# Kernel tuning notes

Hardware: AMD Instinct MI355X
Metric: run time of the kernel (lower is better)

Reference implementation:

```python
import jax, jax.numpy as jnp
import numpy as np

VOCAB, EMB, SEQ, BATCH, UNITS = 10000, 100, 80, 128, 1024


def setup_inputs() -> dict:
    key = jax.random.key(0)
    ks = jax.random.split(key, 12)
    s = lambda k, shape, scale: (jax.random.normal(k, shape, dtype=jnp.float32) * scale)
    inp = {
        'tokens': jax.random.randint(ks[0], (BATCH, SEQ), 0, VOCAB, dtype=jnp.int32),
        'E':   s(ks[1], (VOCAB, EMB), 0.05),
        # GRU cell 1 (input dim = EMB)
        'Wx1': s(ks[2], (EMB, 3 * UNITS), 1.0 / np.sqrt(EMB)),
        'Wh1': s(ks[3], (UNITS, 3 * UNITS), 1.0 / np.sqrt(UNITS)),
        'bx1': jnp.zeros((3 * UNITS,), jnp.float32),
        'bh1': jnp.zeros((3 * UNITS,), jnp.float32),
        # GRU cell 2 (input dim = UNITS)
        'Wx2': s(ks[4], (UNITS, 3 * UNITS), 1.0 / np.sqrt(UNITS)),
        'Wh2': s(ks[5], (UNITS, 3 * UNITS), 1.0 / np.sqrt(UNITS)),
        'bx2': jnp.zeros((3 * UNITS,), jnp.float32),
        'bh2': jnp.zeros((3 * UNITS,), jnp.float32),
        # final dense -> 1 with sigmoid
        'Wf':  s(ks[6], (UNITS, 1), 1.0 / np.sqrt(UNITS)),
        'bf':  jnp.zeros((1,), jnp.float32),
    }
    return inp


def _gru_cell(h, x, Wx, Wh, bx, bh):
    # TF2 keras GRUCell, reset_after=True (inference, no dropout)
    gx = x @ Wx + bx            # [B, 3U]
    gh = h @ Wh + bh            # [B, 3U]
    xz, xr, xn = jnp.split(gx, 3, axis=-1)
    hz, hr, hn = jnp.split(gh, 3, axis=-1)
    z = jax.nn.sigmoid(xz + hz)
    r = jax.nn.sigmoid(xr + hr)
    n = jnp.tanh(xn + r * hn)   # reset_after: r applied AFTER recurrent matmul
    return z * h + (1.0 - z) * n


def reference(tokens, E, Wx1, Wh1, bx1, bh1, Wx2, Wh2, bx2, bh2, Wf, bf):
    x = E[tokens]                         # [B, T, EMB]
    xt = jnp.transpose(x, (1, 0, 2))      # [T, B, EMB] for scan over time
    h0 = jnp.zeros((BATCH, UNITS), x.dtype)
    h1 = jnp.zeros((BATCH, UNITS), x.dtype)

    def step(carry, word):
        h0, h1 = carry
        h0 = _gru_cell(h0, word, Wx1, Wh1, bx1, bh1)
        h1 = _gru_cell(h1, h0,   Wx2, Wh2, bx2, bh2)
        return (h0, h1), None

    (h0, h1), _ = jax.lax.scan(step, (h0, h1), xt)
    return jax.nn.sigmoid(h1 @ Wf + bf)   # [B, 1]
```

## Files before the change

### kernel.cpp

```cpp
#include <hip/hip_runtime.h>
#include <hip/hip_bf16.h>

typedef __bf16 bf16;
typedef __bf16 bf16x8 __attribute__((ext_vector_type(8)));
typedef __bf16 bf16x4 __attribute__((ext_vector_type(4)));
typedef float f32x4 __attribute__((ext_vector_type(4)));

#define T_SEQ 80
#define NB 128
#define NT 1024
#define U 1024
#define U3 3072

#define WT_OFF   0ull
#define WXT_OFF  18874368ull
#define XG_OFF   19660800ull
#define GX1_OFF  22282240ull
#define H0B_OFF  85196800ull
#define H1B_OFF  106430464ull
#define CNT_OFF  127664128ull
#define WS_NEED  127666176ull

#define HBUF_ELEMS 131072ull


#define LDS_SX2_OFF   147456
#define LDS_RED_OFF   (147456 + 24*132*4)
#define LDS_BYTES     (LDS_RED_OFF + 64)

__device__ __forceinline__ float sigmoidf_(float x) { return 1.f / (1.f + __expf(-x)); }

__global__ void k_embed(const int* __restrict__ tok, const float* __restrict__ E,
                        bf16* __restrict__ Xg) {
  int idx = blockIdx.x * 256 + threadIdx.x;
  int k = idx & 127;
  int bt = idx >> 7;
  int b = bt & 127;
  int t = bt >> 7;
  float v = 0.f;
  if (k < 100) v = E[(size_t)tok[b * 80 + t] * 100 + k];
  Xg[idx] = (bf16)v;
}

__global__ void k_trans(const float* __restrict__ Wh1, const float* __restrict__ Wx2,
                        const float* __restrict__ Wh2, bf16* __restrict__ WT) {
  __shared__ float tile[32][33];
  const float* src = (blockIdx.z == 0) ? Wh1 : (blockIdx.z == 1) ? Wx2 : Wh2;
  int cb = blockIdx.x * 32, kb = blockIdx.y * 32;
  int tx = threadIdx.x, ty = threadIdx.y;
  for (int i = ty; i < 32; i += 8) tile[i][tx] = src[(size_t)(kb + i) * U3 + cb + tx];
  __syncthreads();
  bf16* dst = WT + (size_t)blockIdx.z * U3 * U;
  for (int i = ty; i < 32; i += 8) dst[(size_t)(cb + i) * U + kb + tx] = (bf16)tile[tx][i];
}

__global__ void k_wxt(const float* __restrict__ Wx1, bf16* __restrict__ WXT) {
  __shared__ float tile[32][33];
  int cb = blockIdx.x * 32, kb = blockIdx.y * 32;
  int tx = threadIdx.x, ty = threadIdx.y;
  for (int i = ty; i < 32; i += 8) {
    int k = kb + i;
    tile[i][tx] = (k < 100) ? Wx1[(size_t)k * U3 + cb + tx] : 0.f;
  }
  __syncthreads();
  for (int i = ty; i < 32; i += 8) WXT[(size_t)(cb + i) * 128 + kb + tx] = (bf16)tile[tx][i];
}

__global__ __launch_bounds__(256) void k_gx1(const bf16* __restrict__ Xg,
                                             const bf16* __restrict__ WXT,
                                             const float* __restrict__ bx1,
                                             bf16* __restrict__ GX1) {
  int mb = blockIdx.x * 64, nb = blockIdx.y * 64;
  int w = threadIdx.x >> 6, l = threadIdx.x & 63;
  int lr = l & 15, lq = l >> 4;
  int rowA = mb + w * 16 + lr;
  int tA = rowA >> 7, bA = rowA & 127;
  const bf16* aptr = Xg + ((size_t)tA * 128 + bA) * 128 + lq * 8;
  f32x4 acc[4] = {};
  #pragma unroll
  for (int ks = 0; ks < 4; ++ks) {
    bf16x8 a = *(const bf16x8*)(aptr + ks * 32);
    #pragma unroll
    for (int nt = 0; nt < 4; ++nt) {
      int col = nb + nt * 16 + lr;
      bf16x8 b = *(const bf16x8*)(WXT + (size_t)col * 128 + ks * 32 + lq * 8);
      acc[nt] = __builtin_amdgcn_mfma_f32_16x16x32_bf16(a, b, acc[nt], 0, 0, 0);
    }
  }
  int m0 = mb + w * 16 + lq * 4;
  int t0 = m0 >> 7, b0 = m0 & 127;
  #pragma unroll
  for (int nt = 0; nt < 4; ++nt) {
    int col = nb + nt * 16 + lr;
    float bias = bx1[col];
    bf16x4 o;
    #pragma unroll
    for (int j = 0; j < 4; ++j) o[j] = (bf16)(acc[nt][j] + bias);
    *(bf16x4*)(GX1 + ((size_t)t0 * U3 + col) * 128 + b0) = o;
  }
}

__device__ __forceinline__ bf16x8 ldsw(const bf16* Wlds, int sid, int k8) {
  return *(const bf16x8*)(Wlds + ((size_t)sid << 10) + ((k8 ^ (sid & 7) ^ (sid & 8)) << 3));
}

__device__ __forceinline__ void st_pair(bf16* dst_even, int lr, float h) {
  bf16 hb16 = (bf16)h;
  unsigned hb = (unsigned)__builtin_bit_cast(unsigned short, hb16);
  unsigned pb = (unsigned)__shfl_xor((int)hb, 1) & 0xffffu;
  if (!(lr & 1)) {
    unsigned v = hb | (pb << 16);
    __hip_atomic_store((unsigned*)dst_even, v, __ATOMIC_RELAXED, __HIP_MEMORY_SCOPE_AGENT);
  }
}

__device__ void gridbar(int* cnt, int i) {
  __syncthreads();
  if (threadIdx.x == 0) {
    int* gc   = cnt + (blockIdx.x & 7) * 32;
    int* root = cnt + 256;
    int* go   = cnt + 288;
    int old = __hip_atomic_fetch_add(gc, 1, __ATOMIC_RELAXED, __HIP_MEMORY_SCOPE_AGENT);
    if (old == 16 * (i + 1) - 1) {
      int r = __hip_atomic_fetch_add(root, 1, __ATOMIC_RELAXED, __HIP_MEMORY_SCOPE_AGENT);
      if (r == 8 * (i + 1) - 1)
        __hip_atomic_store(go, i + 1, __ATOMIC_RELAXED, __HIP_MEMORY_SCOPE_AGENT);
    }
    while (__hip_atomic_load(go, __ATOMIC_RELAXED, __HIP_MEMORY_SCOPE_AGENT) < i + 1)
      __builtin_amdgcn_s_sleep(4);
  }
  __syncthreads();
}

__global__ __launch_bounds__(NT, 1) void k_main(
    const bf16* __restrict__ WT, const bf16* __restrict__ GX1,
    bf16* __restrict__ h0b, bf16* __restrict__ h1b, int* __restrict__ cnt,
    const float* __restrict__ bh1, const float* __restrict__ bx2,
    const float* __restrict__ bh2, const float* __restrict__ Wf,
    const float* __restrict__ bfp, float* __restrict__ out) {
  extern __shared__ char lds[];
  bf16* Wlds = (bf16*)lds;
  float* Sx2 = (float*)(lds + LDS_SX2_OFF);
  float* red = (float*)(lds + LDS_RED_OFF);

  const int tid = threadIdx.x;
  const int w = tid >> 6, l = tid & 63;
  const int lr = l & 15, lq = l >> 4;
  const int c0 = blockIdx.x * 8;
  const int koff = ((blockIdx.x >> 3) & 15) * 2;

  const int wr_kq = (c0 >> 5) * 512 + (c0 & 31);

  for (int u = tid; u < 9216; u += NT) {
    int chunk = u & 127;
    int sid = u >> 7;
    int mat, gcol;
    if (sid < 16)      { mat = 0; gcol = c0 + (sid & 7) + ((sid >> 3) << 10); }
    else if (sid < 32) { int s = sid - 16; mat = 1; gcol = c0 + (s & 7) + ((s >> 3) << 10); }
    else if (sid < 56) { int s = sid - 32; mat = 2; gcol = c0 + (s & 7) + ((s >> 3) << 10); }
    else               { int s = sid - 56; mat = (s < 8) ? 0 : 1; gcol = 2 * U + c0 + (s & 7); }
    bf16x8 v = *(const bf16x8*)(WT + ((size_t)mat * U3 + gcol) * U + chunk * 8);
    *(bf16x8*)(Wlds + ((size_t)sid << 10) + ((chunk ^ (sid & 7) ^ (sid & 8)) << 3)) = v;
  }
  __syncthreads();

  const int zr_idx = (lr < 8) ? (c0 + lr) : (U + c0 + lr - 8);
  const int n_idx = 2 * U + c0 + (lr & 7);
  const float bzr1 = bh1[zr_idx];
  const float bhn1 = bh1[n_idx];
  const float bzr2 = bx2[zr_idx] + bh2[zr_idx];
  const float bxn2 = bx2[n_idx];
  const float bhn2 = bh2[n_idx];

  float hm[4];
  #pragma unroll
  for (int q = 0; q < 4; ++q) hm[q] = 0.f;

  for (int i = 0; i <= T_SEQ; ++i) {
    const bf16* h0r = h0b + (size_t)i * HBUF_ELEMS;
    const bf16* h1r = h1b + (size_t)(i > 0 ? i - 1 : 0) * HBUF_ELEMS;
    bf16* h0w = h0b + (size_t)(i + 1) * HBUF_ELEMS;
    bf16* h1w = h1b + (size_t)i * HBUF_ELEMS;

    f32x4 a3zr = {}, a3n = {};

    if (w < 8) {
      f32x4 a1zr = {}, a2zr = {}, an = {};

      bf16x4 g4p = {}, gnp = {};
      if (i < T_SEQ) {
        const bf16* gx = GX1 + (size_t)i * U3 * 128;
        int r0 = w * 16 + lq * 4;
        g4p = *(const bf16x4*)(gx + (size_t)zr_idx * 128 + r0);
        gnp = *(const bf16x4*)(gx + (size_t)(2 * U + c0 + (lr & 7)) * 128 + r0);
      }

      const bf16* abase = h0r + w * 16384 + lr * 32 + lq * 8;
      #pragma unroll 8
      for (int ks = 0; ks < 32; ++ks) {
        int kss = (ks + koff) & 31;
        bf16x8 A = *(const bf16x8*)(abase + kss * 512);
        int k8 = kss * 4 + lq;
        bf16x8 B1zr = ldsw(Wlds, lr, k8);
        bf16x8 B2zr = ldsw(Wlds, 16 + lr, k8);
        bf16x8 Bn   = ldsw(Wlds, 56 + lr, k8);
        a1zr = __builtin_amdgcn_mfma_f32_16x16x32_bf16(A, B1zr, a1zr, 0, 0, 0);
        a2zr = __builtin_amdgcn_mfma_f32_16x16x32_bf16(A, B2zr, a2zr, 0, 0, 0);
        an   = __builtin_amdgcn_mfma_f32_16x16x32_bf16(A, Bn,   an,   0, 0, 0);
      }
      {
        int r0 = w * 16 + lq * 4;
        *(f32x4*)(Sx2 + lr * 132 + r0) = a2zr;
        if (lr >= 8) *(f32x4*)(Sx2 + (16 + (lr - 8)) * 132 + r0) = an;
      }
      if (i < T_SEQ) {
        f32x4 sv;
        #pragma unroll
        for (int j = 0; j < 4; ++j) sv[j] = sigmoidf_(a1zr[j] + bzr1 + (float)g4p[j]);
        f32x4 rv;
        #pragma unroll
        for (int j = 0; j < 4; ++j) rv[j] = __shfl_xor(sv[j], 8);
        if (lr < 8) {
          #pragma unroll
          for (int j = 0; j < 4; ++j) {
            float nn = tanhf((float)gnp[j] + rv[j] * (an[j] + bhn1));
            float z = sv[j];
            float h = z * hm[j] + (1.f - z) * nn;
            hm[j] = h;
            st_pair(h0w + w * 16384 + wr_kq + (lq * 4 + j) * 32 + (lr & ~1), lr, h);
          }
        }
      }
    } else if (i > 0) {
      const bf16* abase = h1r + (w - 8) * 16384 + lr * 32 + lq * 8;
      #pragma unroll 8
      for (int ks = 0; ks < 32; ++ks) {
        int kss = (ks + koff) & 31;
        bf16x8 A = *(const bf16x8*)(abase + kss * 512);
        int k8 = kss * 4 + lq;
        bf16x8 B3zr = ldsw(Wlds, 32 + lr, k8);
        bf16x8 B3n  = ldsw(Wlds, 48 + (lr & 7), k8);
        a3zr = __builtin_amdgcn_mfma_f32_16x16x32_bf16(A, B3zr, a3zr, 0, 0, 0);
        a3n  = __builtin_amdgcn_mfma_f32_16x16x32_bf16(A, B3n,  a3n, 0, 0, 0);
      }
    }
    __syncthreads();
    if (w >= 8 && i > 0) {
      int r0 = (w - 8) * 16 + lq * 4;
      f32x4 sv;
      #pragma unroll
      for (int j = 0; j < 4; ++j)
        sv[j] = sigmoidf_(a3zr[j] + bzr2 + Sx2[lr * 132 + r0 + j]);
      f32x4 rv;
      #pragma unroll
      for (int j = 0; j < 4; ++j) rv[j] = __shfl_xor(sv[j], 8);
      if (lr < 8) {
        #pragma unroll
        for (int j = 0; j < 4; ++j) {
          float xn = Sx2[(16 + lr) * 132 + r0 + j] + bxn2;
          float nn = tanhf(xn + rv[j] * (a3n[j] + bhn2));
          float z = sv[j];
          float h = z * hm[j] + (1.f - z) * nn;
          hm[j] = h;
          st_pair(h1w + (w - 8) * 16384 + wr_kq + (lq * 4 + j) * 32 + (lr & ~1), lr, h);
        }
      }
    }
    gridbar(cnt, i);
  }

  {
    const bf16* h1f = h1b + (size_t)T_SEQ * HBUF_ELEMS;
    const int b = blockIdx.x;
    float part = 0.f;
    if (tid < 256) {
      int k0 = tid * 4;
      const bf16* p = h1f + (b >> 4) * 16384 + (k0 >> 5) * 512 + (b & 15) * 32 + (k0 & 31);
      bf16x4 hv = *(const bf16x4*)p;
      #pragma unroll
      for (int j = 0; j < 4; ++j) part += (float)hv[j] * Wf[k0 + j];
    }
    #pragma unroll
    for (int off = 32; off > 0; off >>= 1) part += __shfl_down(part, off);
    if (l == 0) red[w] = part;
    __syncthreads();
    if (tid == 0) {
      float s = bfp[0];
      #pragma unroll
      for (int q = 0; q < 16; ++q) s += red[q];
      out[blockIdx.x] = sigmoidf_(s);
    }
  }
}

extern "C" void kernel_launch(void* const* d_in, const int* in_sizes, int n_in,
                              void* d_out, int out_size, void* d_ws, size_t ws_size,
                              hipStream_t stream) {
  if (ws_size < WS_NEED) return;
  const int*   tok = (const int*)d_in[0];
  const float* E   = (const float*)d_in[1];
  const float* Wx1 = (const float*)d_in[2];
  const float* Wh1 = (const float*)d_in[3];
  const float* bx1 = (const float*)d_in[4];
  const float* bh1 = (const float*)d_in[5];
  const float* Wx2 = (const float*)d_in[6];
  const float* Wh2 = (const float*)d_in[7];
  const float* bx2 = (const float*)d_in[8];
  const float* bh2 = (const float*)d_in[9];
  const float* Wf  = (const float*)d_in[10];
  const float* bfp = (const float*)d_in[11];
  char* ws = (char*)d_ws;
  bf16* WT   = (bf16*)(ws + WT_OFF);
  bf16* WXT  = (bf16*)(ws + WXT_OFF);
  bf16* Xg   = (bf16*)(ws + XG_OFF);
  bf16* GX1  = (bf16*)(ws + GX1_OFF);
  bf16* h0b  = (bf16*)(ws + H0B_OFF);
  bf16* h1b  = (bf16*)(ws + H1B_OFF);
  int*  cnt  = (int*)(ws + CNT_OFF);

  hipMemsetAsync(ws + H0B_OFF, 0, 262144, stream);
  hipMemsetAsync(ws + H1B_OFF, 0, 262144, stream);
  hipMemsetAsync(ws + CNT_OFF, 0, 2048, stream);
  k_embed<<<dim3(5120), dim3(256), 0, stream>>>(tok, E, Xg);
  k_trans<<<dim3(96, 32, 3), dim3(32, 8), 0, stream>>>(Wh1, Wx2, Wh2, WT);
  k_wxt<<<dim3(96, 4), dim3(32, 8), 0, stream>>>(Wx1, WXT);
  k_gx1<<<dim3(160, 48), dim3(256), 0, stream>>>(Xg, WXT, bx1, GX1);
  hipFuncSetAttribute((const void*)k_main, hipFuncAttributeMaxDynamicSharedMemorySize, LDS_BYTES);
  k_main<<<dim3(NB), dim3(NT), LDS_BYTES, stream>>>(WT, GX1, h0b, h1b, cnt,
                                                    bh1, bx2, bh2, Wf, bfp, (float*)d_out);
}
```

Measured before the change: 1.010 ms.

## Halve block threads and give each wave two batch M-tiles for B-fragment reuse

Cuts the persistent block from 1024 to 512 threads (8 waves instead of 16). Each wave now handles two 16-row batch tiles, so every LDS weight fragment it loads feeds two MFMAs. This halves LDS weight reads per MFMA and shrinks the work done at each per-step __syncthreads. The cost is fewer waves to hide the latency of global h loads, more accumulator registers per thread, and more serial MFMA work per wave on each recurrent step.

```diff
diff --git a/kernel.cpp b/kernel.cpp
--- a/kernel.cpp
+++ b/kernel.cpp
@@ -8,7 +8,7 @@
 
 #define T_SEQ 80
 #define NB 128
-#define NT 1024
+#define NT 512
 #define U 1024
 #define U3 3072
 
@@ -172,9 +172,9 @@
   const float bxn2 = bx2[n_idx];
   const float bhn2 = bh2[n_idx];
 
-  float hm[4];
+  float hm[8];
   #pragma unroll
-  for (int q = 0; q < 4; ++q) hm[q] = 0.f;
+  for (int q = 0; q < 8; ++q) hm[q] = 0.f;
 
   for (int i = 0; i <= T_SEQ; ++i) {
     const bf16* h0r = h0b + (size_t)i * HBUF_ELEMS;
@@ -182,87 +182,104 @@
     bf16* h0w = h0b + (size_t)(i + 1) * HBUF_ELEMS;
     bf16* h1w = h1b + (size_t)i * HBUF_ELEMS;
 
-    f32x4 a3zr = {}, a3n = {};
-
-    if (w < 8) {
-      f32x4 a1zr = {}, a2zr = {}, an = {};
-
-      bf16x4 g4p = {}, gnp = {};
+    f32x4 a3zr[2] = {}, a3n[2] = {};
+
+    if (w < 4) {
+      f32x4 a1zr[2] = {}, a2zr[2] = {}, an[2] = {};
+
+      bf16x4 g4p[2] = {}, gnp[2] = {};
       if (i < T_SEQ) {
         const bf16* gx = GX1 + (size_t)i * U3 * 128;
-        int r0 = w * 16 + lq * 4;
-        g4p = *(const bf16x4*)(gx + (size_t)zr_idx * 128 + r0);
-        gnp = *(const bf16x4*)(gx + (size_t)(2 * U + c0 + (lr & 7)) * 128 + r0);
-      }
-
-      const bf16* abase = h0r + w * 16384 + lr * 32 + lq * 8;
+        #pragma unroll
+        for (int mt = 0; mt < 2; ++mt) {
+          int r0 = w * 32 + mt * 16 + lq * 4;
+          g4p[mt] = *(const bf16x4*)(gx + (size_t)zr_idx * 128 + r0);
+          gnp[mt] = *(const bf16x4*)(gx + (size_t)(2 * U + c0 + (lr & 7)) * 128 + r0);
+        }
+      }
+
+      const bf16* abase = h0r + (w * 2) * 16384 + lr * 32 + lq * 8;
       #pragma unroll 8
       for (int ks = 0; ks < 32; ++ks) {
         int kss = (ks + koff) & 31;
-        bf16x8 A = *(const bf16x8*)(abase + kss * 512);
+        bf16x8 A0 = *(const bf16x8*)(abase + kss * 512);
+        bf16x8 A1 = *(const bf16x8*)(abase + 16384 + kss * 512);
         int k8 = kss * 4 + lq;
         bf16x8 B1zr = ldsw(Wlds, lr, k8);
         bf16x8 B2zr = ldsw(Wlds, 16 + lr, k8);
         bf16x8 Bn   = ldsw(Wlds, 56 + lr, k8);
-        a1zr = __builtin_amdgcn_mfma_f32_16x16x32_bf16(A, B1zr, a1zr, 0, 0, 0);
-        a2zr = __builtin_amdgcn_mfma_f32_16x16x32_bf16(A, B2zr, a2zr, 0, 0, 0);
-        an   = __builtin_amdgcn_mfma_f32_16x16x32_bf16(A, Bn,   an,   0, 0, 0);
-      }
-      {
-        int r0 = w * 16 + lq * 4;
-        *(f32x4*)(Sx2 + lr * 132 + r0) = a2zr;
-        if (lr >= 8) *(f32x4*)(Sx2 + (16 + (lr - 8)) * 132 + r0) = an;
+        a1zr[0] = __builtin_amdgcn_mfma_f32_16x16x32_bf16(A0, B1zr, a1zr[0], 0, 0, 0);
+        a2zr[0] = __builtin_amdgcn_mfma_f32_16x16x32_bf16(A0, B2zr, a2zr[0], 0, 0, 0);
+        an[0]   = __builtin_amdgcn_mfma_f32_16x16x32_bf16(A0, Bn,   an[0],   0, 0, 0);
+        a1zr[1] = __builtin_amdgcn_mfma_f32_16x16x32_bf16(A1, B1zr, a1zr[1], 0, 0, 0);
+        a2zr[1] = __builtin_amdgcn_mfma_f32_16x16x32_bf16(A1, B2zr, a2zr[1], 0, 0, 0);
+        an[1]   = __builtin_amdgcn_mfma_f32_16x16x32_bf16(A1, Bn,   an[1],   0, 0, 0);
+      }
+      #pragma unroll
+      for (int mt = 0; mt < 2; ++mt) {
+        int r0 = w * 32 + mt * 16 + lq * 4;
+        *(f32x4*)(Sx2 + lr * 132 + r0) = a2zr[mt];
+        if (lr >= 8) *(f32x4*)(Sx2 + (16 + (lr - 8)) * 132 + r0) = an[mt];
       }
       if (i < T_SEQ) {
+        #pragma unroll
+        for (int mt = 0; mt < 2; ++mt) {
+          f32x4 sv;
+          #pragma unroll
+          for (int j = 0; j < 4; ++j) sv[j] = sigmoidf_(a1zr[mt][j] + bzr1 + (float)g4p[mt][j]);
+          f32x4 rv;
+          #pragma unroll
+          for (int j = 0; j < 4; ++j) rv[j] = __shfl_xor(sv[j], 8);
+          if (lr < 8) {
+            #pragma unroll
+            for (int j = 0; j < 4; ++j) {
+              float nn = tanhf((float)gnp[mt][j] + rv[j] * (an[mt][j] + bhn1));
+              float z = sv[j];
+              float h = z * hm[mt * 4 + j] + (1.f - z) * nn;
+              hm[mt * 4 + j] = h;
+              st_pair(h0w + (w * 2 + mt) * 16384 + wr_kq + (lq * 4 + j) * 32 + (lr & ~1), lr, h);
+            }
+          }
+        }
+      }
+    } else if (i > 0) {
+      const bf16* abase = h1r + ((w - 4) * 2) * 16384 + lr * 32 + lq * 8;
+      #pragma unroll 8
+      for (int ks = 0; ks < 32; ++ks) {
+        int kss = (ks + koff) & 31;
+        bf16x8 A0 = *(const bf16x8*)(abase + kss * 512);
+        bf16x8 A1 = *(const bf16x8*)(abase + 16384 + kss * 512);
+        int k8 = kss * 4 + lq;
+        bf16x8 B3zr = ldsw(Wlds, 32 + lr, k8);
+        bf16x8 B3n  = ldsw(Wlds, 48 + (lr & 7), k8);
+        a3zr[0] = __builtin_amdgcn_mfma_f32_16x16x32_bf16(A0, B3zr, a3zr[0], 0, 0, 0);
+        a3n[0]  = __builtin_amdgcn_mfma_f32_16x16x32_bf16(A0, B3n,  a3n[0], 0, 0, 0);
+        a3zr[1] = __builtin_amdgcn_mfma_f32_16x16x32_bf16(A1, B3zr, a3zr[1], 0, 0, 0);
+        a3n[1]  = __builtin_amdgcn_mfma_f32_16x16x32_bf16(A1, B3n,  a3n[1], 0, 0, 0);
+      }
+    }
+    __syncthreads();
+    if (w >= 4 && i > 0) {
+      #pragma unroll
+      for (int mt = 0; mt < 2; ++mt) {
+        int r0 = (w - 4) * 32 + mt * 16 + lq * 4;
         f32x4 sv;
         #pragma unroll
-        for (int j = 0; j < 4; ++j) sv[j] = sigmoidf_(a1zr[j] + bzr1 + (float)g4p[j]);
+        for (int j = 0; j < 4; ++j)
+          sv[j] = sigmoidf_(a3zr[mt][j] + bzr2 + Sx2[lr * 132 + r0 + j]);
         f32x4 rv;
         #pragma unroll
         for (int j = 0; j < 4; ++j) rv[j] = __shfl_xor(sv[j], 8);
         if (lr < 8) {
           #pragma unroll
           for (int j = 0; j < 4; ++j) {
-            float nn = tanhf((float)gnp[j] + rv[j] * (an[j] + bhn1));
+            float xn = Sx2[(16 + lr) * 132 + r0 + j] + bxn2;
+            float nn = tanhf(xn + rv[j] * (a3n[mt][j] + bhn2));
             float z = sv[j];
-            float h = z * hm[j] + (1.f - z) * nn;
-            hm[j] = h;
-            st_pair(h0w + w * 16384 + wr_kq + (lq * 4 + j) * 32 + (lr & ~1), lr, h);
+            float h = z * hm[mt * 4 + j] + (1.f - z) * nn;
+            hm[mt * 4 + j] = h;
+            st_pair(h1w + ((w - 4) * 2 + mt) * 16384 + wr_kq + (lq * 4 + j) * 32 + (lr & ~1), lr, h);
           }
-        }
-      }
-    } else if (i > 0) {
-      const bf16* abase = h1r + (w - 8) * 16384 + lr * 32 + lq * 8;
-      #pragma unroll 8
-      for (int ks = 0; ks < 32; ++ks) {
-        int kss = (ks + koff) & 31;
-        bf16x8 A = *(const bf16x8*)(abase + kss * 512);
-        int k8 = kss * 4 + lq;
-        bf16x8 B3zr = ldsw(Wlds, 32 + lr, k8);
-        bf16x8 B3n  = ldsw(Wlds, 48 + (lr & 7), k8);
-        a3zr = __builtin_amdgcn_mfma_f32_16x16x32_bf16(A, B3zr, a3zr, 0, 0, 0);
-        a3n  = __builtin_amdgcn_mfma_f32_16x16x32_bf16(A, B3n,  a3n, 0, 0, 0);
-      }
-    }
-    __syncthreads();
-    if (w >= 8 && i > 0) {
-      int r0 = (w - 8) * 16 + lq * 4;
-      f32x4 sv;
-      #pragma unroll
-      for (int j = 0; j < 4; ++j)
-        sv[j] = sigmoidf_(a3zr[j] + bzr2 + Sx2[lr * 132 + r0 + j]);
-      f32x4 rv;
-      #pragma unroll
-      for (int j = 0; j < 4; ++j) rv[j] = __shfl_xor(sv[j], 8);
-      if (lr < 8) {
-        #pragma unroll
-        for (int j = 0; j < 4; ++j) {
-          float xn = Sx2[(16 + lr) * 132 + r0 + j] + bxn2;
-          float nn = tanhf(xn + rv[j] * (a3n[j] + bhn2));
-          float z = sv[j];
-          float h = z * hm[j] + (1.f - z) * nn;
-          hm[j] = h;
-          st_pair(h1w + (w - 8) * 16384 + wr_kq + (lq * 4 + j) * 32 + (lr & ~1), lr, h);
         }
       }
     }
@@ -287,7 +304,7 @@
     if (tid == 0) {
       float s = bfp[0];
       #pragma unroll
-      for (int q = 0; q < 16; ++q) s += red[q];
+      for (int q = 0; q < 8; ++q) s += red[q];
       out[blockIdx.x] = sigmoidf_(s);
     }
   }
```

After: 1.263 ms. 1.25x slower.

## Split hidden units across 256 blocks with 4 columns each and packed z/r/n tiles

Applied to the files above, without the earlier changes.

Doubles the persistent grid from 128 to 256 blocks, so each block owns 4 hidden units instead of 8. The z, r and n gate columns are packed into one 16-wide MFMA tile, with 4 columns repeated as padding, and the n-gate values are fetched with lane shuffles. This halves per-block LDS weights and cuts the MFMA count per step from 5 to 3. The cost is a larger grid barrier (32 arrivals per group), some wasted padded MFMA columns, and a dependence on all 256 blocks being co-resident.

```diff
diff --git a/kernel.cpp b/kernel.cpp
--- a/kernel.cpp
+++ b/kernel.cpp
@@ -7,7 +7,7 @@
 typedef float f32x4 __attribute__((ext_vector_type(4)));
 
 #define T_SEQ 80
-#define NB 128
+#define NB 256
 #define NT 1024
 #define U 1024
 #define U3 3072
@@ -24,8 +24,8 @@
 #define HBUF_ELEMS 131072ull
 
 
-#define LDS_SX2_OFF   147456
-#define LDS_RED_OFF   (147456 + 24*132*4)
+#define LDS_SX2_OFF   73728
+#define LDS_RED_OFF   (73728 + 12*132*4)
 #define LDS_BYTES     (LDS_RED_OFF + 64)
 
 __device__ __forceinline__ float sigmoidf_(float x) { return 1.f / (1.f + __expf(-x)); }
@@ -100,8 +100,8 @@
   }
 }
 
-__device__ __forceinline__ bf16x8 ldsw(const bf16* Wlds, int sid, int k8) {
-  return *(const bf16x8*)(Wlds + ((size_t)sid << 10) + ((k8 ^ (sid & 7) ^ (sid & 8)) << 3));
+__device__ __forceinline__ bf16x8 ldsw(const bf16* Wlds, int mat, int scol, int k8) {
+  return *(const bf16x8*)(Wlds + (((mat * 12 + scol) << 10) + ((k8 ^ scol) << 3)));
 }
 
 __device__ __forceinline__ void st_pair(bf16* dst_even, int lr, float h) {
@@ -121,7 +121,7 @@
     int* root = cnt + 256;
     int* go   = cnt + 288;
     int old = __hip_atomic_fetch_add(gc, 1, __ATOMIC_RELAXED, __HIP_MEMORY_SCOPE_AGENT);
-    if (old == 16 * (i + 1) - 1) {
+    if (old == 32 * (i + 1) - 1) {
       int r = __hip_atomic_fetch_add(root, 1, __ATOMIC_RELAXED, __HIP_MEMORY_SCOPE_AGENT);
       if (r == 8 * (i + 1) - 1)
         __hip_atomic_store(go, i + 1, __ATOMIC_RELAXED, __HIP_MEMORY_SCOPE_AGENT);
@@ -146,31 +146,31 @@
   const int tid = threadIdx.x;
   const int w = tid >> 6, l = tid & 63;
   const int lr = l & 15, lq = l >> 4;
-  const int c0 = blockIdx.x * 8;
-  const int koff = ((blockIdx.x >> 3) & 15) * 2;
+  const int c0 = blockIdx.x * 4;
+  const int koff = (blockIdx.x >> 3) & 31;
+  const int scol = (lr < 12) ? lr : (lr - 12);
+
+  int col_g;
+  if (lr < 4)       col_g = c0 + lr;
+  else if (lr < 8)  col_g = U + c0 + (lr - 4);
+  else if (lr < 12) col_g = 2 * U + c0 + (lr - 8);
+  else              col_g = c0 + (lr - 12);
 
   const int wr_kq = (c0 >> 5) * 512 + (c0 & 31);
 
-  for (int u = tid; u < 9216; u += NT) {
+  for (int u = tid; u < 4608; u += NT) {
     int chunk = u & 127;
     int sid = u >> 7;
-    int mat, gcol;
-    if (sid < 16)      { mat = 0; gcol = c0 + (sid & 7) + ((sid >> 3) << 10); }
-    else if (sid < 32) { int s = sid - 16; mat = 1; gcol = c0 + (s & 7) + ((s >> 3) << 10); }
-    else if (sid < 56) { int s = sid - 32; mat = 2; gcol = c0 + (s & 7) + ((s >> 3) << 10); }
-    else               { int s = sid - 56; mat = (s < 8) ? 0 : 1; gcol = 2 * U + c0 + (s & 7); }
+    int mat = sid / 12, s = sid - mat * 12;
+    int gcol = (s < 4) ? (c0 + s) : (s < 8) ? (U + c0 + s - 4) : (2 * U + c0 + s - 8);
     bf16x8 v = *(const bf16x8*)(WT + ((size_t)mat * U3 + gcol) * U + chunk * 8);
-    *(bf16x8*)(Wlds + ((size_t)sid << 10) + ((chunk ^ (sid & 7) ^ (sid & 8)) << 3)) = v;
-  }
-  __syncthreads();
-
-  const int zr_idx = (lr < 8) ? (c0 + lr) : (U + c0 + lr - 8);
-  const int n_idx = 2 * U + c0 + (lr & 7);
-  const float bzr1 = bh1[zr_idx];
-  const float bhn1 = bh1[n_idx];
-  const float bzr2 = bx2[zr_idx] + bh2[zr_idx];
-  const float bxn2 = bx2[n_idx];
-  const float bhn2 = bh2[n_idx];
+    *(bf16x8*)(Wlds + ((size_t)sid << 10) + ((chunk ^ s) << 3)) = v;
+  }
+  __syncthreads();
+
+  const float b1c  = bh1[col_g];
+  const float bx2c = bx2[col_g];
+  const float bh2c = bh2[col_g];
 
   float hm[4];
   #pragma unroll
@@ -182,17 +182,16 @@
     bf16* h0w = h0b + (size_t)(i + 1) * HBUF_ELEMS;
     bf16* h1w = h1b + (size_t)i * HBUF_ELEMS;
 
-    f32x4 a3zr = {}, a3n = {};
+    f32x4 a3 = {};
 
     if (w < 8) {
-      f32x4 a1zr = {}, a2zr = {}, an = {};
-
-      bf16x4 g4p = {}, gnp = {};
+      f32x4 a1 = {}, a2 = {};
+
+      bf16x4 g4 = {};
       if (i < T_SEQ) {
         const bf16* gx = GX1 + (size_t)i * U3 * 128;
         int r0 = w * 16 + lq * 4;
-        g4p = *(const bf16x4*)(gx + (size_t)zr_idx * 128 + r0);
-        gnp = *(const bf16x4*)(gx + (size_t)(2 * U + c0 + (lr & 7)) * 128 + r0);
+        g4 = *(const bf16x4*)(gx + (size_t)col_g * 128 + r0);
       }
 
       const bf16* abase = h0r + w * 16384 + lr * 32 + lq * 8;
@@ -201,29 +200,35 @@
         int kss = (ks + koff) & 31;
         bf16x8 A = *(const bf16x8*)(abase + kss * 512);
         int k8 = kss * 4 + lq;
-        bf16x8 B1zr = ldsw(Wlds, lr, k8);
-        bf16x8 B2zr = ldsw(Wlds, 16 + lr, k8);
-        bf16x8 Bn   = ldsw(Wlds, 56 + lr, k8);
-        a1zr = __builtin_amdgcn_mfma_f32_16x16x32_bf16(A, B1zr, a1zr, 0, 0, 0);
-        a2zr = __builtin_amdgcn_mfma_f32_16x16x32_bf16(A, B2zr, a2zr, 0, 0, 0);
-        an   = __builtin_amdgcn_mfma_f32_16x16x32_bf16(A, Bn,   an,   0, 0, 0);
+        bf16x8 B1 = ldsw(Wlds, 0, scol, k8);
+        bf16x8 B2 = ldsw(Wlds, 1, scol, k8);
+        a1 = __builtin_amdgcn_mfma_f32_16x16x32_bf16(A, B1, a1, 0, 0, 0);
+        a2 = __builtin_amdgcn_mfma_f32_16x16x32_bf16(A, B2, a2, 0, 0, 0);
       }
       {
         int r0 = w * 16 + lq * 4;
-        *(f32x4*)(Sx2 + lr * 132 + r0) = a2zr;
-        if (lr >= 8) *(f32x4*)(Sx2 + (16 + (lr - 8)) * 132 + r0) = an;
+        if (lr < 12) *(f32x4*)(Sx2 + lr * 132 + r0) = a2;
       }
       if (i < T_SEQ) {
-        f32x4 sv;
+        f32x4 gf, p, q, sv;
         #pragma unroll
-        for (int j = 0; j < 4; ++j) sv[j] = sigmoidf_(a1zr[j] + bzr1 + (float)g4p[j]);
-        f32x4 rv;
+        for (int j = 0; j < 4; ++j) {
+          gf[j] = (float)g4[j];
+          p[j] = a1[j] + b1c;
+          q[j] = p[j] + gf[j];
+          sv[j] = sigmoidf_(q[j]);
+        }
+        f32x4 rv, gn, pn;
         #pragma unroll
-        for (int j = 0; j < 4; ++j) rv[j] = __shfl_xor(sv[j], 8);
-        if (lr < 8) {
+        for (int j = 0; j < 4; ++j) {
+          rv[j] = __shfl_xor(sv[j], 4);
+          gn[j] = __shfl_xor(gf[j], 8);
+          pn[j] = __shfl_xor(p[j], 8);
+        }
+        if (lr < 4) {
           #pragma unroll
           for (int j = 0; j < 4; ++j) {
-            float nn = tanhf((float)gnp[j] + rv[j] * (an[j] + bhn1));
+            float nn = tanhf(gn[j] + rv[j] * pn[j]);
             float z = sv[j];
             float h = z * hm[j] + (1.f - z) * nn;
             hm[j] = h;
@@ -238,27 +243,33 @@
         int kss = (ks + koff) & 31;
         bf16x8 A = *(const bf16x8*)(abase + kss * 512);
         int k8 = kss * 4 + lq;
-        bf16x8 B3zr = ldsw(Wlds, 32 + lr, k8);
-        bf16x8 B3n  = ldsw(Wlds, 48 + (lr & 7), k8);
-        a3zr = __builtin_amdgcn_mfma_f32_16x16x32_bf16(A, B3zr, a3zr, 0, 0, 0);
-        a3n  = __builtin_amdgcn_mfma_f32_16x16x32_bf16(A, B3n,  a3n, 0, 0, 0);
+        bf16x8 B3 = ldsw(Wlds, 2, scol, k8);
+        a3 = __builtin_amdgcn_mfma_f32_16x16x32_bf16(A, B3, a3, 0, 0, 0);
       }
     }
     __syncthreads();
     if (w >= 8 && i > 0) {
       int r0 = (w - 8) * 16 + lq * 4;
-      f32x4 sv;
+      f32x4 s2 = *(const f32x4*)(Sx2 + scol * 132 + r0);
+      f32x4 q, p3, xn, sv;
       #pragma unroll
-      for (int j = 0; j < 4; ++j)
-        sv[j] = sigmoidf_(a3zr[j] + bzr2 + Sx2[lr * 132 + r0 + j]);
-      f32x4 rv;
+      for (int j = 0; j < 4; ++j) {
+        q[j]  = a3[j] + bx2c + bh2c + s2[j];
+        p3[j] = a3[j] + bh2c;
+        xn[j] = s2[j] + bx2c;
+        sv[j] = sigmoidf_(q[j]);
+      }
+      f32x4 rv, hn, xnn;
       #pragma unroll
-      for (int j = 0; j < 4; ++j) rv[j] = __shfl_xor(sv[j], 8);
-      if (lr < 8) {
+      for (int j = 0; j < 4; ++j) {
+        rv[j]  = __shfl_xor(sv[j], 4);
+        hn[j]  = __shfl_xor(p3[j], 8);
+        xnn[j] = __shfl_xor(xn[j], 8);
+      }
+      if (lr < 4) {
         #pragma unroll
         for (int j = 0; j < 4; ++j) {
-          float xn = Sx2[(16 + lr) * 132 + r0 + j] + bxn2;
-          float nn = tanhf(xn + rv[j] * (a3n[j] + bhn2));
+          float nn = tanhf(xnn[j] + rv[j] * hn[j]);
           float z = sv[j];
           float h = z * hm[j] + (1.f - z) * nn;
           hm[j] = h;
@@ -269,7 +280,7 @@
     gridbar(cnt, i);
   }
 
-  {
+  if (blockIdx.x < 128) {
     const bf16* h1f = h1b + (size_t)T_SEQ * HBUF_ELEMS;
     const int b = blockIdx.x;
     float part = 0.f;
```

New measurement: 1.009 ms. About the same (-0.1%).
